# Kernel tuning notes

Measured on AMD Instinct MI355X. Metric: run time of the kernel, lower is better.

## Reference

```python
import jax, jax.numpy as jnp
import numpy as np

H = 8        # hidden_size
T = 609      # seq_size
IN = 5       # input feature dim
B = 2048     # batch


def _lstm_layer(x, Wih, Whh, bih, bhh):
    """PyTorch-compatible single-layer LSTM, batch_first. x: [B, T, I].
    Gate order i, f, g, o; zero initial (h, c)."""
    b = x.shape[0]
    h_dim = Wih.shape[0] // 4
    bias = bih + bhh

    def step(carry, xt):
        h, c = carry
        gates = xt @ Wih.T + h @ Whh.T + bias          # [B, 4H]
        i, f, g, o = jnp.split(gates, 4, axis=-1)
        i = jax.nn.sigmoid(i)
        f = jax.nn.sigmoid(f)
        g = jnp.tanh(g)
        o = jax.nn.sigmoid(o)
        c = f * c + i * g
        h = o * jnp.tanh(c)
        return (h, c), h

    h0 = jnp.zeros((b, h_dim), x.dtype)
    (_, _), ys = jax.lax.scan(step, (h0, h0), jnp.swapaxes(x, 0, 1))  # ys: [T, B, H]
    return jnp.swapaxes(ys, 0, 1)                                      # [B, T, H]


def setup_inputs() -> dict:
    key = jax.random.key(0)
    ks = jax.random.split(key, 20)
    s_lstm = 1.0 / np.sqrt(H)   # PyTorch LSTM init scale

    def u(k, shape, s):
        return jax.random.uniform(k, shape, jnp.float32, -s, s)

    inp = {"x": jax.random.normal(ks[0], (B, T, IN), jnp.float32)}
    # LSTM layer 1 (input 5), layers 2-3 (input H)
    ins = [IN, H, H]
    for l in range(3):
        k0, k1, k2, k3 = jax.random.split(ks[1 + l], 4)
        inp[f"Wih{l+1}"] = u(k0, (4 * H, ins[l]), s_lstm)
        inp[f"Whh{l+1}"] = u(k1, (4 * H, H), s_lstm)
        inp[f"bih{l+1}"] = u(k2, (4 * H,), s_lstm)
        inp[f"bhh{l+1}"] = u(k3, (4 * H,), s_lstm)
    # MLP head
    d_in = H * T  # 4872
    dims = [(4096, d_in), (1024, 4096), (T, 1024)]
    for i, (o, ii) in enumerate(dims):
        s = 1.0 / np.sqrt(ii)
        k0, k1 = jax.random.split(ks[10 + i], 2)
        inp[f"W{i+1}"] = u(k0, (o, ii), s)
        inp[f"b{i+1}"] = u(k1, (o,), s)
    return inp


def reference(x, Wih1, Whh1, bih1, bhh1, Wih2, Whh2, bih2, bhh2,
              Wih3, Whh3, bih3, bhh3, W1, b1, W2, b2, W3, b3):
    out = _lstm_layer(x, Wih1, Whh1, bih1, bhh1)
    out = _lstm_layer(out, Wih2, Whh2, bih2, bhh2)
    out = _lstm_layer(out, Wih3, Whh3, bih3, bhh3)
    out = out.reshape(x.shape[0], -1)              # [B, T*H]
    out = jax.nn.relu(out @ W1.T + b1)
    out = jax.nn.relu(out @ W2.T + b2)
    out = out @ W3.T + b3                          # [B, T]
    return out
```

## Files before the change

kernel.cpp:

```cpp
#include <hip/hip_runtime.h>
#include <hip/hip_bf16.h>

typedef __attribute__((ext_vector_type(8))) short short8;
typedef __attribute__((ext_vector_type(4))) float floatx4;
typedef unsigned short u16;

#define T_SZ 609
#define K1V  4872
#define K1P  4896
#define RD   4

static __device__ __forceinline__ u16 f2bf(float f) {
    union { float f; unsigned u; } a; a.f = f;
    unsigned r = a.u + 0x7FFF + ((a.u >> 16) & 1);
    return (u16)(r >> 16);
}

static __device__ __forceinline__ void gload_lds16(const u16* g, u16* l) {
    __builtin_amdgcn_global_load_lds(
        (const __attribute__((address_space(1))) void*)g,
        (__attribute__((address_space(3))) void*)l, 16, 0, 0);
}

#define WG_LOAD(p)     __hip_atomic_load((p), __ATOMIC_ACQUIRE, __HIP_MEMORY_SCOPE_WORKGROUP)
#define WG_STORE(p, v) __hip_atomic_store((p), (v), __ATOMIC_RELEASE, __HIP_MEMORY_SCOPE_WORKGROUP)

__global__ __launch_bounds__(256) void cvt_kernel(const float* __restrict__ s,
                                                  u16* __restrict__ d, int n) {
    int i = (blockIdx.x * 256 + threadIdx.x) * 8;
    if (i < n) {
        float4 a = *(const float4*)(s + i);
        float4 b = *(const float4*)(s + i + 4);
        u16 o[8] = { f2bf(a.x), f2bf(a.y), f2bf(a.z), f2bf(a.w),
                     f2bf(b.x), f2bf(b.y), f2bf(b.z), f2bf(b.w) };
        *(uint4*)(d + i) = *(const uint4*)o;
    }
}

__global__ __launch_bounds__(256) void cvt_pad_kernel(const float* __restrict__ s,
                                                      u16* __restrict__ d,
                                                      int R, int K, int Kp) {
    int chunk = blockIdx.x * 256 + threadIdx.x;
    int cpr = Kp >> 3;
    int r = chunk / cpr;
    int c = (chunk - r * cpr) << 3;
    u16 o[8] = {0, 0, 0, 0, 0, 0, 0, 0};
    if (r < R && c < K) {
        const float* p = s + (size_t)r * K + c;
        float4 a = *(const float4*)p;
        float4 b = *(const float4*)(p + 4);
        o[0] = f2bf(a.x); o[1] = f2bf(a.y); o[2] = f2bf(a.z); o[3] = f2bf(a.w);
        o[4] = f2bf(b.x); o[5] = f2bf(b.y); o[6] = f2bf(b.z); o[7] = f2bf(b.w);
    }
    *(uint4*)&d[(size_t)r * Kp + c] = *(const uint4*)o;
}

__global__ __launch_bounds__(192) void lstm3_kernel(
    const float* __restrict__ x,
    const float* __restrict__ Wih1, const float* __restrict__ Whh1,
    const float* __restrict__ bih1, const float* __restrict__ bhh1,
    const float* __restrict__ Wih2, const float* __restrict__ Whh2,
    const float* __restrict__ bih2, const float* __restrict__ bhh2,
    const float* __restrict__ Wih3, const float* __restrict__ Whh3,
    const float* __restrict__ bih3, const float* __restrict__ bhh3,
    u16* __restrict__ A1)
{
    __shared__ __align__(16) float xs[2 * T_SZ * 5];
    __shared__ __align__(16) float r1[RD * 16], r2[RD * 16], r3[RD * 16];
    __shared__ int p1, p2, c2, c3;

    const int tid = threadIdx.x;
    const int b0  = blockIdx.x * 2;

    const float* xg = x + (size_t)b0 * (T_SZ * 5);
    for (int i = tid; i < 2 * T_SZ * 5; i += 192) xs[i] = xg[i];
    if (tid == 0) { p1 = 0; p2 = 0; c2 = 0; c3 = 0; }
    if (tid < 48) {
        int r = tid / 24, c = tid - r * 24;
        A1[(size_t)(b0 + r) * K1P + K1V + c] = 0;
    }
    __syncthreads();

    const int lane = tid & 63, wid = tid >> 6;
    const int gi   = lane & 31;
    const int rh   = lane >> 5;
    const int jj   = gi & 7;
    const int gt   = gi >> 3;
    const int base = lane & 32;

    const float am = (gt == 2) ? -2.f : -1.f;
    const float aa = (gt == 2) ?  2.f :  1.f;
    const float ab = (gt == 2) ? -1.f :  0.f;

    auto lstep = [&](float a, float& c) -> float {
        float e = __expf(am * a);
        float v = __builtin_fmaf(aa, __fdividef(1.f, 1.f + e), ab);
        float vi = __shfl(v, base + jj,      64);
        float vf = __shfl(v, base + 8 + jj,  64);
        float vg = __shfl(v, base + 16 + jj, 64);
        float vo = __shfl(v, base + 24 + jj, 64);
        c = __builtin_fmaf(vf, c, vi * vg);
        float ec = __expf(-2.f * __builtin_fabsf(c));
        float th = (1.f - ec) * __fdividef(1.f, 1.f + ec);
        return vo * __builtin_copysignf(th, c);
    };

    auto dot8 = [&](const float* hp, const float* w, float& a, float& b) {
        float4 h0 = *(const float4*)hp;
        float4 h1 = *(const float4*)(hp + 4);
        a = __builtin_fmaf(w[0], h0.x, a); b = __builtin_fmaf(w[1], h0.y, b);
        a = __builtin_fmaf(w[2], h0.z, a); b = __builtin_fmaf(w[3], h0.w, b);
        a = __builtin_fmaf(w[4], h1.x, a); b = __builtin_fmaf(w[5], h1.y, b);
        a = __builtin_fmaf(w[6], h1.z, a); b = __builtin_fmaf(w[7], h1.w, b);
    };

    if (wid == 0) {
        float wi[5], wh[8];
#pragma unroll
        for (int k = 0; k < 5; ++k) wi[k] = Wih1[gi * 5 + k];
#pragma unroll
        for (int k = 0; k < 8; ++k) wh[k] = Whh1[gi * 8 + k];
        const float bs = bih1[gi] + bhh1[gi];
        const float* xr = &xs[rh * (T_SZ * 5)];
        float cst = 0.f;
        for (int t = 0; t < T_SZ; ++t) {
            float a = bs, b = 0.f;
#pragma unroll
            for (int k = 0; k < 5; ++k) a = __builtin_fmaf(wi[k], xr[t * 5 + k], a);
            if (t > 0) dot8(&r1[((t - 1) & (RD - 1)) * 16 + rh * 8], wh, a, b);
            float h = lstep(a + b, cst);
            if (t >= RD) while (WG_LOAD(&c2) < t - (RD - 1)) {}
            if (gi < 8) r1[(t & (RD - 1)) * 16 + rh * 8 + jj] = h;
            if (lane == 0) WG_STORE(&p1, t + 1);
        }
    } else if (wid == 1) {
        float wi[8], wh[8];
#pragma unroll
        for (int k = 0; k < 8; ++k) { wi[k] = Wih2[gi * 8 + k]; wh[k] = Whh2[gi * 8 + k]; }
        const float bs = bih2[gi] + bhh2[gi];
        float cst = 0.f;
        for (int t = 0; t < T_SZ; ++t) {
            while (WG_LOAD(&p1) < t + 1) {}
            float a = bs, b = 0.f;
            dot8(&r1[(t & (RD - 1)) * 16 + rh * 8], wi, a, b);
            if (lane == 0) WG_STORE(&c2, t + 1);
            if (t > 0) dot8(&r2[((t - 1) & (RD - 1)) * 16 + rh * 8], wh, a, b);
            float h = lstep(a + b, cst);
            if (t >= RD) while (WG_LOAD(&c3) < t - (RD - 1)) {}
            if (gi < 8) r2[(t & (RD - 1)) * 16 + rh * 8 + jj] = h;
            if (lane == 0) WG_STORE(&p2, t + 1);
        }
    } else {
        float wi[8], wh[8];
#pragma unroll
        for (int k = 0; k < 8; ++k) { wi[k] = Wih3[gi * 8 + k]; wh[k] = Whh3[gi * 8 + k]; }
        const float bs = bih3[gi] + bhh3[gi];
        float cst = 0.f;
        u16* outp = A1 + (size_t)(b0 + rh) * K1P;
        for (int t = 0; t < T_SZ; ++t) {
            while (WG_LOAD(&p2) < t + 1) {}
            float a = bs, b = 0.f;
            dot8(&r2[(t & (RD - 1)) * 16 + rh * 8], wi, a, b);
            if (lane == 0) WG_STORE(&c3, t + 1);
            if (t > 0) dot8(&r3[((t - 1) & (RD - 1)) * 16 + rh * 8], wh, a, b);
            float h = lstep(a + b, cst);
            if (gi < 8) {
                r3[(t & (RD - 1)) * 16 + rh * 8 + jj] = h;
                outp[t * 8 + jj] = f2bf(h);
            }
        }
    }
}

template<int BM, int BN, bool RELU, bool NGUARD, bool OUTF32>
__global__ __launch_bounds__(256) void gemm_bt(
    const u16* __restrict__ A, int lda,
    const u16* __restrict__ B, int ldb,
    const float* __restrict__ bias,
    void* __restrict__ Cv, int ldc, int N, int K)
{
    constexpr int WM = BM / 2, WN = BN / 2;
    constexpr int TM = WM / 16, TN = WN / 16;
    __shared__ u16 As[BM * 32];
    __shared__ u16 Bs[BN * 32];

    const int tid = threadIdx.x;
    const int bm  = blockIdx.y * BM;
    const int bn  = blockIdx.x * BN;
    const int l   = tid & 63, w = tid >> 6;
    const int wr  = w >> 1, wc = w & 1;
    const int lr  = l & 15, q = l >> 4;
    const int lrow = l >> 2;
    const int lcol = (l & 3) << 3;

    floatx4 acc[TM][TN];
#pragma unroll
    for (int i = 0; i < TM; ++i)
#pragma unroll
        for (int j = 0; j < TN; ++j) acc[i][j] = (floatx4){0.f, 0.f, 0.f, 0.f};

    const u16* Ab = A + (size_t)bm * lda;
    const u16* Bb = B + (size_t)bn * ldb;

    for (int k0 = 0; k0 < K; k0 += 32) {
#pragma unroll
        for (int i = 0; i < BM / 64; ++i) {
            int r0 = w * (BM / 4) + i * 16;
            gload_lds16(Ab + (size_t)(r0 + lrow) * lda + k0 + lcol, &As[r0 * 32]);
        }
#pragma unroll
        for (int i = 0; i < BN / 64; ++i) {
            int r0 = w * (BN / 4) + i * 16;
            gload_lds16(Bb + (size_t)(r0 + lrow) * ldb + k0 + lcol, &Bs[r0 * 32]);
        }
        __syncthreads();

        short8 fa[TM], fb[TN];
#pragma unroll
        for (int i = 0; i < TM; ++i)
            fa[i] = *(const short8*)&As[(wr * WM + i * 16 + lr) * 32 + q * 8];
#pragma unroll
        for (int j = 0; j < TN; ++j)
            fb[j] = *(const short8*)&Bs[(wc * WN + j * 16 + lr) * 32 + q * 8];
#pragma unroll
        for (int i = 0; i < TM; ++i)
#pragma unroll
            for (int j = 0; j < TN; ++j)
                acc[i][j] = __builtin_amdgcn_mfma_f32_16x16x32_bf16(fa[i], fb[j], acc[i][j], 0, 0, 0);
        __syncthreads();
    }

#pragma unroll
    for (int j = 0; j < TN; ++j) {
        int n = bn + wc * WN + j * 16 + lr;
        bool nok = (!NGUARD) || (n < N);
        float bv = nok ? bias[n] : 0.f;
#pragma unroll
        for (int i = 0; i < TM; ++i) {
            int m0r = bm + wr * WM + i * 16 + q * 4;
#pragma unroll
            for (int r = 0; r < 4; ++r) {
                float vv = acc[i][j][r] + bv;
                if (RELU) vv = fmaxf(vv, 0.f);
                if (nok) {
                    size_t idx = (size_t)(m0r + r) * ldc + n;
                    if (OUTF32) ((float*)Cv)[idx] = vv;
                    else        ((u16*)Cv)[idx] = f2bf(vv);
                }
            }
        }
    }
}

extern "C" void kernel_launch(void* const* d_in, const int* in_sizes, int n_in,
                              void* d_out, int out_size, void* d_ws, size_t ws_size,
                              hipStream_t stream)
{
    const float* x    = (const float*)d_in[0];
    const float* Wih1 = (const float*)d_in[1];
    const float* Whh1 = (const float*)d_in[2];
    const float* bih1 = (const float*)d_in[3];
    const float* bhh1 = (const float*)d_in[4];
    const float* Wih2 = (const float*)d_in[5];
    const float* Whh2 = (const float*)d_in[6];
    const float* bih2 = (const float*)d_in[7];
    const float* bhh2 = (const float*)d_in[8];
    const float* Wih3 = (const float*)d_in[9];
    const float* Whh3 = (const float*)d_in[10];
    const float* bih3 = (const float*)d_in[11];
    const float* bhh3 = (const float*)d_in[12];
    const float* W1 = (const float*)d_in[13];
    const float* b1 = (const float*)d_in[14];
    const float* W2 = (const float*)d_in[15];
    const float* b2 = (const float*)d_in[16];
    const float* W3 = (const float*)d_in[17];
    const float* b3 = (const float*)d_in[18];

    u16* A1  = (u16*)d_ws;
    u16* A2  = A1  + (size_t)2048 * K1P;
    u16* A3  = A2  + (size_t)2048 * 4096;
    u16* W1b = A3  + (size_t)2048 * 1024;
    u16* W2b = W1b + (size_t)4096 * K1P;
    u16* W3b = W2b + (size_t)1024 * 4096;

    cvt_pad_kernel<<<9792, 256, 0, stream>>>(W1, W1b, 4096, K1V, K1P);
    cvt_kernel<<<2048, 256, 0, stream>>>(W2, W2b, 1024 * 4096);
    cvt_pad_kernel<<<320, 256, 0, stream>>>(W3, W3b, T_SZ, 1024, 1024);

    lstm3_kernel<<<1024, 192, 0, stream>>>(x, Wih1, Whh1, bih1, bhh1,
                                           Wih2, Whh2, bih2, bhh2,
                                           Wih3, Whh3, bih3, bhh3, A1);

    gemm_bt<128, 128, true, false, false><<<dim3(32, 16), 256, 0, stream>>>(
        A1, K1P, W1b, K1P, b1, A2, 4096, 4096, K1P);

    gemm_bt<64, 128, true, false, false><<<dim3(8, 32), 256, 0, stream>>>(
        A2, 4096, W2b, 4096, b2, A3, 1024, 1024, 4096);

    gemm_bt<64, 128, false, true, true><<<dim3(5, 32), 256, 0, stream>>>(
        A3, 1024, W3b, 1024, b3, d_out, T_SZ, T_SZ, 1024);
}
```

Measured before the change: 698.4 us.

## Rewrite LSTM as single-wave kernel with per-unit lanes and DPP broadcasts

Replaces the three-wave pipelined LSTM, which passed hidden states between layers through LDS with spin-wait flags, with a single 64-lane wave per block. Each lane owns one hidden unit of one batch row and computes all four gates for it, and the hidden vector is shared within an 8-lane group using DPP butterfly permutes. This removes the LDS handoffs, the atomic flag polling and the cross-lane shuffles. In exchange all three layers run serially inside each time step on one wave, only 256 waves are launched, and the register footprint grows because every lane holds the weights of all three layers.

```diff
diff --git a/kernel.cpp b/kernel.cpp
--- a/kernel.cpp
+++ b/kernel.cpp
@@ -8,7 +8,6 @@
 #define T_SZ 609
 #define K1V  4872
 #define K1P  4896
-#define RD   4
 
 static __device__ __forceinline__ u16 f2bf(float f) {
     union { float f; unsigned u; } a; a.f = f;
@@ -21,9 +20,6 @@
         (const __attribute__((address_space(1))) void*)g,
         (__attribute__((address_space(3))) void*)l, 16, 0, 0);
 }
-
-#define WG_LOAD(p)     __hip_atomic_load((p), __ATOMIC_ACQUIRE, __HIP_MEMORY_SCOPE_WORKGROUP)
-#define WG_STORE(p, v) __hip_atomic_store((p), (v), __ATOMIC_RELEASE, __HIP_MEMORY_SCOPE_WORKGROUP)
 
 __global__ __launch_bounds__(256) void cvt_kernel(const float* __restrict__ s,
                                                   u16* __restrict__ d, int n) {
@@ -55,7 +51,44 @@
     *(uint4*)&d[(size_t)r * Kp + c] = *(const uint4*)o;
 }
 
-__global__ __launch_bounds__(192) void lstm3_kernel(
+
+template<int CTRL>
+static __device__ __forceinline__ float dppf(float v) {
+    union { float f; int i; } a, b;
+    a.f = v;
+    b.i = __builtin_amdgcn_update_dpp(0, a.i, CTRL, 0xF, 0xF, true);
+    return b.f;
+}
+
+static __device__ __forceinline__ void bfly(float v, float* o) {
+    o[0] = v;
+    o[1] = dppf<0xB1>(v);
+    o[2] = dppf<0x4E>(v);
+    o[3] = dppf<0x1B>(v);
+    float m7 = dppf<0x141>(v);
+    o[7] = m7;
+    o[6] = dppf<0xB1>(m7);
+    o[5] = dppf<0x4E>(m7);
+    o[4] = dppf<0x1B>(m7);
+}
+
+static __device__ __forceinline__ float dot8(const float* w, const float* v, float s0) {
+    float a = s0, b = 0.f;
+#pragma unroll
+    for (int m = 0; m < 4; ++m) a = __builtin_fmaf(w[m], v[m], a);
+#pragma unroll
+    for (int m = 4; m < 8; ++m) b = __builtin_fmaf(w[m], v[m], b);
+    return a + b;
+}
+
+static __device__ __forceinline__ float sigm(float a) {
+    return __fdividef(1.f, 1.f + __expf(-a));
+}
+static __device__ __forceinline__ float tns(float a) {
+    return __builtin_fmaf(2.f, __fdividef(1.f, 1.f + __expf(-2.f * a)), -1.f);
+}
+
+__global__ __launch_bounds__(64) void lstm3_kernel(
     const float* __restrict__ x,
     const float* __restrict__ Wih1, const float* __restrict__ Whh1,
     const float* __restrict__ bih1, const float* __restrict__ bhh1,
@@ -65,110 +98,91 @@
     const float* __restrict__ bih3, const float* __restrict__ bhh3,
     u16* __restrict__ A1)
 {
-    __shared__ __align__(16) float xs[2 * T_SZ * 5];
-    __shared__ __align__(16) float r1[RD * 16], r2[RD * 16], r3[RD * 16];
-    __shared__ int p1, p2, c2, c3;
-
-    const int tid = threadIdx.x;
-    const int b0  = blockIdx.x * 2;
-
-    const float* xg = x + (size_t)b0 * (T_SZ * 5);
-    for (int i = tid; i < 2 * T_SZ * 5; i += 192) xs[i] = xg[i];
-    if (tid == 0) { p1 = 0; p2 = 0; c2 = 0; c3 = 0; }
-    if (tid < 48) {
-        int r = tid / 24, c = tid - r * 24;
-        A1[(size_t)(b0 + r) * K1P + K1V + c] = 0;
-    }
-    __syncthreads();
-
-    const int lane = tid & 63, wid = tid >> 6;
-    const int gi   = lane & 31;
-    const int rh   = lane >> 5;
-    const int jj   = gi & 7;
-    const int gt   = gi >> 3;
-    const int base = lane & 32;
-
-    const float am = (gt == 2) ? -2.f : -1.f;
-    const float aa = (gt == 2) ?  2.f :  1.f;
-    const float ab = (gt == 2) ? -1.f :  0.f;
-
-    auto lstep = [&](float a, float& c) -> float {
-        float e = __expf(am * a);
-        float v = __builtin_fmaf(aa, __fdividef(1.f, 1.f + e), ab);
-        float vi = __shfl(v, base + jj,      64);
-        float vf = __shfl(v, base + 8 + jj,  64);
-        float vg = __shfl(v, base + 16 + jj, 64);
-        float vo = __shfl(v, base + 24 + jj, 64);
-        c = __builtin_fmaf(vf, c, vi * vg);
-        float ec = __expf(-2.f * __builtin_fabsf(c));
-        float th = (1.f - ec) * __fdividef(1.f, 1.f + ec);
-        return vo * __builtin_copysignf(th, c);
-    };
-
-    auto dot8 = [&](const float* hp, const float* w, float& a, float& b) {
-        float4 h0 = *(const float4*)hp;
-        float4 h1 = *(const float4*)(hp + 4);
-        a = __builtin_fmaf(w[0], h0.x, a); b = __builtin_fmaf(w[1], h0.y, b);
-        a = __builtin_fmaf(w[2], h0.z, a); b = __builtin_fmaf(w[3], h0.w, b);
-        a = __builtin_fmaf(w[4], h1.x, a); b = __builtin_fmaf(w[5], h1.y, b);
-        a = __builtin_fmaf(w[6], h1.z, a); b = __builtin_fmaf(w[7], h1.w, b);
-    };
-
-    if (wid == 0) {
-        float wi[5], wh[8];
-#pragma unroll
-        for (int k = 0; k < 5; ++k) wi[k] = Wih1[gi * 5 + k];
-#pragma unroll
-        for (int k = 0; k < 8; ++k) wh[k] = Whh1[gi * 8 + k];
-        const float bs = bih1[gi] + bhh1[gi];
-        const float* xr = &xs[rh * (T_SZ * 5)];
-        float cst = 0.f;
-        for (int t = 0; t < T_SZ; ++t) {
-            float a = bs, b = 0.f;
-#pragma unroll
-            for (int k = 0; k < 5; ++k) a = __builtin_fmaf(wi[k], xr[t * 5 + k], a);
-            if (t > 0) dot8(&r1[((t - 1) & (RD - 1)) * 16 + rh * 8], wh, a, b);
-            float h = lstep(a + b, cst);
-            if (t >= RD) while (WG_LOAD(&c2) < t - (RD - 1)) {}
-            if (gi < 8) r1[(t & (RD - 1)) * 16 + rh * 8 + jj] = h;
-            if (lane == 0) WG_STORE(&p1, t + 1);
-        }
-    } else if (wid == 1) {
-        float wi[8], wh[8];
-#pragma unroll
-        for (int k = 0; k < 8; ++k) { wi[k] = Wih2[gi * 8 + k]; wh[k] = Whh2[gi * 8 + k]; }
-        const float bs = bih2[gi] + bhh2[gi];
-        float cst = 0.f;
-        for (int t = 0; t < T_SZ; ++t) {
-            while (WG_LOAD(&p1) < t + 1) {}
-            float a = bs, b = 0.f;
-            dot8(&r1[(t & (RD - 1)) * 16 + rh * 8], wi, a, b);
-            if (lane == 0) WG_STORE(&c2, t + 1);
-            if (t > 0) dot8(&r2[((t - 1) & (RD - 1)) * 16 + rh * 8], wh, a, b);
-            float h = lstep(a + b, cst);
-            if (t >= RD) while (WG_LOAD(&c3) < t - (RD - 1)) {}
-            if (gi < 8) r2[(t & (RD - 1)) * 16 + rh * 8 + jj] = h;
-            if (lane == 0) WG_STORE(&p2, t + 1);
-        }
-    } else {
-        float wi[8], wh[8];
-#pragma unroll
-        for (int k = 0; k < 8; ++k) { wi[k] = Wih3[gi * 8 + k]; wh[k] = Whh3[gi * 8 + k]; }
-        const float bs = bih3[gi] + bhh3[gi];
-        float cst = 0.f;
-        u16* outp = A1 + (size_t)(b0 + rh) * K1P;
-        for (int t = 0; t < T_SZ; ++t) {
-            while (WG_LOAD(&p2) < t + 1) {}
-            float a = bs, b = 0.f;
-            dot8(&r2[(t & (RD - 1)) * 16 + rh * 8], wi, a, b);
-            if (lane == 0) WG_STORE(&c3, t + 1);
-            if (t > 0) dot8(&r3[((t - 1) & (RD - 1)) * 16 + rh * 8], wh, a, b);
-            float h = lstep(a + b, cst);
-            if (gi < 8) {
-                r3[(t & (RD - 1)) * 16 + rh * 8 + jj] = h;
-                outp[t * 8 + jj] = f2bf(h);
-            }
-        }
+    const int lane = threadIdx.x & 63;
+    const int u = lane & 7;
+    const int r = lane >> 3;
+    const int b0 = blockIdx.x * 8;
+    const int row = b0 + r;
+
+    {
+        int idx = lane;
+#pragma unroll
+        for (int it = 0; it < 3; ++it, idx += 64) {
+            int rr = idx / 24, cc = idx - rr * 24;
+            A1[(size_t)(b0 + rr) * K1P + K1V + cc] = 0;
+        }
+    }
+
+    float wi1[4][8], wh1[4][8], wi2[4][8], wh2[4][8], wi3[4][8], wh3[4][8];
+    float bs1[4], bs2[4], bs3[4];
+#pragma unroll
+    for (int g = 0; g < 4; ++g) {
+        const int G = g * 8 + u;
+        bs1[g] = bih1[G] + bhh1[G];
+        bs2[g] = bih2[G] + bhh2[G];
+        bs3[g] = bih3[G] + bhh3[G];
+#pragma unroll
+        for (int m = 0; m < 8; ++m) {
+            const int k = u ^ m;
+            wh1[g][m] = Whh1[G * 8 + k];
+            wi1[g][m] = (k < 5) ? Wih1[G * 5 + k] : 0.f;
+            wi2[g][m] = Wih2[G * 8 + k];
+            wh2[g][m] = Whh2[G * 8 + k];
+            wi3[g][m] = Wih3[G * 8 + k];
+            wh3[g][m] = Whh3[G * 8 + k];
+        }
+    }
+
+    const float* xrow = x + (size_t)row * (T_SZ * 5);
+    const int ux = (u < 5) ? u : 0;
+    u16* outp = A1 + (size_t)row * K1P;
+
+    float h1v[8], h2v[8], h3v[8];
+#pragma unroll
+    for (int m = 0; m < 8; ++m) { h1v[m] = 0.f; h2v[m] = 0.f; h3v[m] = 0.f; }
+    float c1 = 0.f, c2 = 0.f, c3 = 0.f;
+    float xc = xrow[ux];
+
+#pragma unroll 1
+    for (int t = 0; t < T_SZ; ++t) {
+        const int tn = (t < T_SZ - 1) ? t + 1 : t;
+        const float xn = xrow[tn * 5 + ux];
+
+        float q1[4], q2[4], q3[4];
+#pragma unroll
+        for (int g = 0; g < 4; ++g) {
+            q1[g] = dot8(wh1[g], h1v, bs1[g]);
+            q2[g] = dot8(wh2[g], h2v, bs2[g]);
+            q3[g] = dot8(wh3[g], h3v, bs3[g]);
+        }
+
+        float xv[8];
+        bfly(xc, xv);
+
+#pragma unroll
+        for (int g = 0; g < 4; ++g) q1[g] = dot8(wi1[g], xv, q1[g]);
+        {
+            float i = sigm(q1[0]), f = sigm(q1[1]), gg = tns(q1[2]), o = sigm(q1[3]);
+            c1 = __builtin_fmaf(f, c1, i * gg);
+            bfly(o * tns(c1), h1v);
+        }
+#pragma unroll
+        for (int g = 0; g < 4; ++g) q2[g] = dot8(wi2[g], h1v, q2[g]);
+        {
+            float i = sigm(q2[0]), f = sigm(q2[1]), gg = tns(q2[2]), o = sigm(q2[3]);
+            c2 = __builtin_fmaf(f, c2, i * gg);
+            bfly(o * tns(c2), h2v);
+        }
+#pragma unroll
+        for (int g = 0; g < 4; ++g) q3[g] = dot8(wi3[g], h2v, q3[g]);
+        {
+            float i = sigm(q3[0]), f = sigm(q3[1]), gg = tns(q3[2]), o = sigm(q3[3]);
+            c3 = __builtin_fmaf(f, c3, i * gg);
+            float h = o * tns(c3);
+            bfly(h, h3v);
+            outp[t * 8 + u] = f2bf(h);
+        }
+        xc = xn;
     }
 }
 
@@ -287,9 +301,9 @@
     cvt_kernel<<<2048, 256, 0, stream>>>(W2, W2b, 1024 * 4096);
     cvt_pad_kernel<<<320, 256, 0, stream>>>(W3, W3b, T_SZ, 1024, 1024);
 
-    lstm3_kernel<<<1024, 192, 0, stream>>>(x, Wih1, Whh1, bih1, bhh1,
-                                           Wih2, Whh2, bih2, bhh2,
-                                           Wih3, Whh3, bih3, bhh3, A1);
+    lstm3_kernel<<<256, 64, 0, stream>>>(x, Wih1, Whh1, bih1, bhh1,
+                                         Wih2, Whh2, bih2, bhh2,
+                                         Wih3, Whh3, bih3, bhh3, A1);
 
     gemm_bt<128, 128, true, false, false><<<dim3(32, 16), 256, 0, stream>>>(
         A1, K1P, W1b, K1P, b1, A2, 4096, 4096, K1P);
```

After: 1.008 ms. 1.44x slower.

## Fuse weight conversion into LSTM launch and deepen GEMM K-tile to 64

Applied to the files above, without the earlier changes.

The three fp32-to-bf16 weight conversion kernels are folded into the LSTM kernel as 256 extra blocks. These run alongside the latency-bound LSTM recurrence blocks, hiding the conversion traffic and removing launch gaps. The GEMM now stages a 64-wide K slice per barrier pair with two MFMA sub-steps, which halves the number of syncs, and K1P is padded to a multiple of 64 to match. The last GEMM uses 64x64 tiles for more blocks. Doubled LDS per block may reduce occupancy, and the conversion blocks compete with the LSTM blocks for CUs.

```diff
diff --git a/kernel.cpp b/kernel.cpp
--- a/kernel.cpp
+++ b/kernel.cpp
@@ -7,7 +7,7 @@
 
 #define T_SZ 609
 #define K1V  4872
-#define K1P  4896
+#define K1P  4928
 #define RD   4
 
 static __device__ __forceinline__ u16 f2bf(float f) {
@@ -25,37 +25,18 @@
 #define WG_LOAD(p)     __hip_atomic_load((p), __ATOMIC_ACQUIRE, __HIP_MEMORY_SCOPE_WORKGROUP)
 #define WG_STORE(p, v) __hip_atomic_store((p), (v), __ATOMIC_RELEASE, __HIP_MEMORY_SCOPE_WORKGROUP)
 
-__global__ __launch_bounds__(256) void cvt_kernel(const float* __restrict__ s,
-                                                  u16* __restrict__ d, int n) {
-    int i = (blockIdx.x * 256 + threadIdx.x) * 8;
-    if (i < n) {
-        float4 a = *(const float4*)(s + i);
-        float4 b = *(const float4*)(s + i + 4);
-        u16 o[8] = { f2bf(a.x), f2bf(a.y), f2bf(a.z), f2bf(a.w),
-                     f2bf(b.x), f2bf(b.y), f2bf(b.z), f2bf(b.w) };
-        *(uint4*)(d + i) = *(const uint4*)o;
-    }
-}
-
-__global__ __launch_bounds__(256) void cvt_pad_kernel(const float* __restrict__ s,
-                                                      u16* __restrict__ d,
-                                                      int R, int K, int Kp) {
-    int chunk = blockIdx.x * 256 + threadIdx.x;
-    int cpr = Kp >> 3;
-    int r = chunk / cpr;
-    int c = (chunk - r * cpr) << 3;
-    u16 o[8] = {0, 0, 0, 0, 0, 0, 0, 0};
-    if (r < R && c < K) {
-        const float* p = s + (size_t)r * K + c;
-        float4 a = *(const float4*)p;
-        float4 b = *(const float4*)(p + 4);
-        o[0] = f2bf(a.x); o[1] = f2bf(a.y); o[2] = f2bf(a.z); o[3] = f2bf(a.w);
-        o[4] = f2bf(b.x); o[5] = f2bf(b.y); o[6] = f2bf(b.z); o[7] = f2bf(b.w);
-    }
-    *(uint4*)&d[(size_t)r * Kp + c] = *(const uint4*)o;
-}
-
-__global__ __launch_bounds__(192) void lstm3_kernel(
+static __device__ __forceinline__ void cvt8(const float* __restrict__ p, u16* __restrict__ d) {
+    float4 a = *(const float4*)p;
+    float4 b = *(const float4*)(p + 4);
+    u16 o[8] = { f2bf(a.x), f2bf(a.y), f2bf(a.z), f2bf(a.w),
+                 f2bf(b.x), f2bf(b.y), f2bf(b.z), f2bf(b.w) };
+    *(uint4*)d = *(const uint4*)o;
+}
+static __device__ __forceinline__ void zero8(u16* __restrict__ d) {
+    *(uint4*)d = (uint4){0, 0, 0, 0};
+}
+
+__global__ __launch_bounds__(192) void lstm3_fused(
     const float* __restrict__ x,
     const float* __restrict__ Wih1, const float* __restrict__ Whh1,
     const float* __restrict__ bih1, const float* __restrict__ bhh1,
@@ -63,8 +44,29 @@
     const float* __restrict__ bih2, const float* __restrict__ bhh2,
     const float* __restrict__ Wih3, const float* __restrict__ Whh3,
     const float* __restrict__ bih3, const float* __restrict__ bhh3,
-    u16* __restrict__ A1)
+    u16* __restrict__ A1,
+    const float* __restrict__ W1, u16* __restrict__ W1b,
+    const float* __restrict__ W2, u16* __restrict__ W2b,
+    const float* __restrict__ W3, u16* __restrict__ W3b)
 {
+    if (blockIdx.x >= 1024) {
+        const int ct = (blockIdx.x - 1024) * 192 + threadIdx.x;
+        const int cs = 256 * 192;
+        for (int i = ct; i < 4096 * 616; i += cs) {
+            int r = i / 616, c = (i - r * 616) << 3;
+            u16* d = W1b + (size_t)r * K1P + c;
+            if (c < K1V) cvt8(W1 + (size_t)r * K1V + c, d); else zero8(d);
+        }
+        for (int i = ct; i < 524288; i += cs)
+            cvt8(W2 + (size_t)i * 8, W2b + (size_t)i * 8);
+        for (int i = ct; i < 640 * 128; i += cs) {
+            int r = i >> 7, c = (i & 127) << 3;
+            u16* d = W3b + (size_t)r * 1024 + c;
+            if (r < T_SZ) cvt8(W3 + (size_t)r * 1024 + c, d); else zero8(d);
+        }
+        return;
+    }
+
     __shared__ __align__(16) float xs[2 * T_SZ * 5];
     __shared__ __align__(16) float r1[RD * 16], r2[RD * 16], r3[RD * 16];
     __shared__ int p1, p2, c2, c3;
@@ -75,8 +77,8 @@
     const float* xg = x + (size_t)b0 * (T_SZ * 5);
     for (int i = tid; i < 2 * T_SZ * 5; i += 192) xs[i] = xg[i];
     if (tid == 0) { p1 = 0; p2 = 0; c2 = 0; c3 = 0; }
-    if (tid < 48) {
-        int r = tid / 24, c = tid - r * 24;
+    if (tid < 112) {
+        int r = tid / 56, c = tid - r * 56;
         A1[(size_t)(b0 + r) * K1P + K1V + c] = 0;
     }
     __syncthreads();
@@ -181,8 +183,8 @@
 {
     constexpr int WM = BM / 2, WN = BN / 2;
     constexpr int TM = WM / 16, TN = WN / 16;
-    __shared__ u16 As[BM * 32];
-    __shared__ u16 Bs[BN * 32];
+    __shared__ u16 As[BM * 64];
+    __shared__ u16 Bs[BN * 64];
 
     const int tid = threadIdx.x;
     const int bm  = blockIdx.y * BM;
@@ -190,8 +192,8 @@
     const int l   = tid & 63, w = tid >> 6;
     const int wr  = w >> 1, wc = w & 1;
     const int lr  = l & 15, q = l >> 4;
-    const int lrow = l >> 2;
-    const int lcol = (l & 3) << 3;
+    const int lrow = l >> 3;
+    const int lcol = (l & 7) << 3;
 
     floatx4 acc[TM][TN];
 #pragma unroll
@@ -202,31 +204,34 @@
     const u16* Ab = A + (size_t)bm * lda;
     const u16* Bb = B + (size_t)bn * ldb;
 
-    for (int k0 = 0; k0 < K; k0 += 32) {
-#pragma unroll
-        for (int i = 0; i < BM / 64; ++i) {
-            int r0 = w * (BM / 4) + i * 16;
-            gload_lds16(Ab + (size_t)(r0 + lrow) * lda + k0 + lcol, &As[r0 * 32]);
-        }
-#pragma unroll
-        for (int i = 0; i < BN / 64; ++i) {
-            int r0 = w * (BN / 4) + i * 16;
-            gload_lds16(Bb + (size_t)(r0 + lrow) * ldb + k0 + lcol, &Bs[r0 * 32]);
+    for (int k0 = 0; k0 < K; k0 += 64) {
+#pragma unroll
+        for (int i = 0; i < BM / 32; ++i) {
+            int r0 = w * (BM / 4) + i * 8;
+            gload_lds16(Ab + (size_t)(r0 + lrow) * lda + k0 + lcol, &As[r0 * 64]);
+        }
+#pragma unroll
+        for (int i = 0; i < BN / 32; ++i) {
+            int r0 = w * (BN / 4) + i * 8;
+            gload_lds16(Bb + (size_t)(r0 + lrow) * ldb + k0 + lcol, &Bs[r0 * 64]);
         }
         __syncthreads();
 
-        short8 fa[TM], fb[TN];
-#pragma unroll
-        for (int i = 0; i < TM; ++i)
-            fa[i] = *(const short8*)&As[(wr * WM + i * 16 + lr) * 32 + q * 8];
-#pragma unroll
-        for (int j = 0; j < TN; ++j)
-            fb[j] = *(const short8*)&Bs[(wc * WN + j * 16 + lr) * 32 + q * 8];
-#pragma unroll
-        for (int i = 0; i < TM; ++i)
+#pragma unroll
+        for (int ks = 0; ks < 2; ++ks) {
+            short8 fa[TM], fb[TN];
+#pragma unroll
+            for (int i = 0; i < TM; ++i)
+                fa[i] = *(const short8*)&As[(wr * WM + i * 16 + lr) * 64 + ks * 32 + q * 8];
 #pragma unroll
             for (int j = 0; j < TN; ++j)
-                acc[i][j] = __builtin_amdgcn_mfma_f32_16x16x32_bf16(fa[i], fb[j], acc[i][j], 0, 0, 0);
+                fb[j] = *(const short8*)&Bs[(wc * WN + j * 16 + lr) * 64 + ks * 32 + q * 8];
+#pragma unroll
+            for (int i = 0; i < TM; ++i)
+#pragma unroll
+                for (int j = 0; j < TN; ++j)
+                    acc[i][j] = __builtin_amdgcn_mfma_f32_16x16x32_bf16(fa[i], fb[j], acc[i][j], 0, 0, 0);
+        }
         __syncthreads();
     }
 
@@ -283,13 +288,10 @@
     u16* W2b = W1b + (size_t)4096 * K1P;
     u16* W3b = W2b + (size_t)1024 * 4096;
 
-    cvt_pad_kernel<<<9792, 256, 0, stream>>>(W1, W1b, 4096, K1V, K1P);
-    cvt_kernel<<<2048, 256, 0, stream>>>(W2, W2b, 1024 * 4096);
-    cvt_pad_kernel<<<320, 256, 0, stream>>>(W3, W3b, T_SZ, 1024, 1024);
-
-    lstm3_kernel<<<1024, 192, 0, stream>>>(x, Wih1, Whh1, bih1, bhh1,
-                                           Wih2, Whh2, bih2, bhh2,
-                                           Wih3, Whh3, bih3, bhh3, A1);
+    lstm3_fused<<<1280, 192, 0, stream>>>(x, Wih1, Whh1, bih1, bhh1,
+                                          Wih2, Whh2, bih2, bhh2,
+                                          Wih3, Whh3, bih3, bhh3, A1,
+                                          W1, W1b, W2, W2b, W3, W3b);
 
     gemm_bt<128, 128, true, false, false><<<dim3(32, 16), 256, 0, stream>>>(
         A1, K1P, W1b, K1P, b1, A2, 4096, 4096, K1P);
@@ -297,6 +299,6 @@
     gemm_bt<64, 128, true, false, false><<<dim3(8, 32), 256, 0, stream>>>(
         A2, 4096, W2b, 4096, b2, A3, 1024, 1024, 4096);
 
-    gemm_bt<64, 128, false, true, true><<<dim3(5, 32), 256, 0, stream>>>(
+    gemm_bt<64, 64, false, true, true><<<dim3(10, 32), 256, 0, stream>>>(
         A3, 1024, W3b, 1024, b3, d_out, T_SZ, T_SZ, 1024);
 }
```

New measurement: 641.7 us. 8.1% less time.
